# Optimization experiments

Hardware: AMD Instinct MI355X
Metric: run time of the kernel (lower is better)

The kernel has to match this reference:

```python
import jax, jax.numpy as jnp
import numpy as np

EPS = 1e-5

def layer_norm(x, gamma, beta):
    mu = jnp.mean(x, axis=-1, keepdims=True)
    var = jnp.mean(jnp.square(x - mu), axis=-1, keepdims=True)
    return (x - mu) * jax.lax.rsqrt(var + EPS) * gamma + beta

def setup_inputs() -> dict:
    key = jax.random.key(0)
    ks = jax.random.split(key, 12)
    B, S, D = 2, 4096, 1024
    H = 4 * D
    s_in = 1.0 / np.sqrt(D)
    s_h = 1.0 / np.sqrt(H)
    return {
        "input_embedding": jax.random.normal(ks[0], (B, S, D), dtype=jnp.float32),
        "Wq": jax.random.uniform(ks[1], (D, D), jnp.float32, -s_in, s_in),
        "bq": jax.random.uniform(ks[2], (D,), jnp.float32, -s_in, s_in),
        "Wk": jax.random.uniform(ks[3], (D, D), jnp.float32, -s_in, s_in),
        "bk": jax.random.uniform(ks[4], (D,), jnp.float32, -s_in, s_in),
        "Wv": jax.random.uniform(ks[5], (D, D), jnp.float32, -s_in, s_in),
        "bv": jax.random.uniform(ks[6], (D,), jnp.float32, -s_in, s_in),
        "W1": jax.random.uniform(ks[7], (D, H), jnp.float32, -s_in, s_in),
        "b1": jax.random.uniform(ks[8], (H,), jnp.float32, -s_in, s_in),
        "W2": jax.random.uniform(ks[9], (H, D), jnp.float32, -s_h, s_h),
        "b2": jax.random.uniform(ks[10], (D,), jnp.float32, -s_h, s_h),
        "gamma": jnp.ones((D,), jnp.float32),
        "beta": jnp.zeros((D,), jnp.float32),
    }

def reference(input_embedding, Wq, bq, Wk, bk, Wv, bv, W1, b1, W2, b2, gamma, beta):
    D = input_embedding.shape[-1]
    # projections
    k = input_embedding @ Wk + bk
    q = input_embedding @ Wq + bq
    v = input_embedding @ Wv + bv
    # NOTE: original calls attention(k, q, v) so Q<-k, K<-q, V<-v (faithful quirk)
    scores = jnp.einsum('bsd,btd->bst', k, q) / jnp.sqrt(jnp.float32(D))
    attn = jax.nn.softmax(scores, axis=-1)
    attn_out = jnp.einsum('bst,btd->bsd', attn, v)  # dropout = identity (eval)
    x = layer_norm(input_embedding + attn_out, gamma, beta)
    # feed-forward (GELU exact, dropout identity)
    h = jax.nn.gelu(x @ W1 + b1, approximate=False)
    ff = h @ W2 + b2
    return layer_norm(x + ff, gamma, beta)
```

## Files before the change

kernel.cpp:

```cpp
#include <hip/hip_runtime.h>
#include <hip/hip_bf16.h>
#include <stdint.h>

#define AS1 __attribute__((address_space(1)))
#define AS3 __attribute__((address_space(3)))

typedef __bf16 bf16x8 __attribute__((ext_vector_type(8)));
typedef __bf16 bf16x4 __attribute__((ext_vector_type(4)));
typedef float  f32x4  __attribute__((ext_vector_type(4)));

__device__ __forceinline__ void gld_lds16(const void* g, void* l) {
    __builtin_amdgcn_global_load_lds((AS1 void*)g, (AS3 void*)l, 16, 0, 0);
}

__device__ __forceinline__ void xcd_remap(int& bc, int& br) {
    const int GX = gridDim.x, GY = gridDim.y;
    const int L = blockIdx.y * GX + blockIdx.x;
    int rw, rh, nregx;
    if (GX >= 16 && (GX & 1) == 0 && (GY & 3) == 0) {
        rw = GX >> 1; rh = GY >> 2; nregx = 2;
    } else if ((GY & 7) == 0) {
        rw = GX;      rh = GY >> 3; nregx = 1;
    } else {
        bc = blockIdx.x; br = blockIdx.y; return;
    }
    const int xcd  = L & 7;
    const int slot = L >> 3;
    const int rx = xcd % nregx, ry = xcd / nregx;
    bc = rx * rw + slot % rw;
    br = ry * rh + slot / rw;
}

__global__ __launch_bounds__(256, 4)
void gemm_nt(const __bf16* __restrict__ A, const __bf16* __restrict__ B,
             __bf16* __restrict__ C, const float* __restrict__ bias,
             int K, int lda, int ldb, int ldc,
             long sA, long sB, long sC, long sBias,
             int ep, float scale)
{
    __shared__ __bf16 smA[2][4096];
    __shared__ __bf16 smB[2][4096];
    const int t  = threadIdx.x;
    const int l  = t & 63;
    const int w  = t >> 6;
    const int wm = w >> 1, wn = w & 1;
    const int lr = l & 15;
    const int lq = l >> 4;
    const long bz = blockIdx.z;
    int br, bc;
    xcd_remap(bc, br);

    const int swc = ((t & 3) ^ ((t >> 3) & 3)) * 8;
    const __bf16* ag = A + bz * sA + (size_t)(br * 128 + (t >> 2)) * lda + swc;
    const __bf16* bg = B + bz * sB + (size_t)(bc * 128 + (t >> 2)) * ldb + swc;
    const size_t a64 = (size_t)64 * lda, b64 = (size_t)64 * ldb;

    f32x4 acc[4][4];
    const f32x4 zero4 = {0.f, 0.f, 0.f, 0.f};
#pragma unroll
    for (int i = 0; i < 4; ++i)
#pragma unroll
        for (int j = 0; j < 4; ++j) acc[i][j] = zero4;

    const int paOff = (wm * 64 + lr) * 32 + ((lq ^ ((lr >> 1) & 3)) * 8);
    const int pbOff = (wn * 64 + lr) * 32 + ((lq ^ ((lr >> 1) & 3)) * 8);

    auto prefetch = [&](int b) {
        __bf16* la = &smA[b][t * 8];
        __bf16* lb = &smB[b][t * 8];
        gld_lds16(ag,       la);
        gld_lds16(ag + a64, la + 2048);
        gld_lds16(bg,       lb);
        gld_lds16(bg + b64, lb + 2048);
        ag += 32; bg += 32;
    };
    auto compute = [&](int b) {
        const __bf16* pa = &smA[b][paOff];
        const __bf16* pb = &smB[b][pbOff];
        bf16x8 af[4], bfr[4];
#pragma unroll
        for (int i = 0; i < 4; ++i) af[i]  = *(const bf16x8*)(pa + i * 16 * 32);
#pragma unroll
        for (int j = 0; j < 4; ++j) bfr[j] = *(const bf16x8*)(pb + j * 16 * 32);
#pragma unroll
        for (int i = 0; i < 4; ++i)
#pragma unroll
            for (int j = 0; j < 4; ++j)
                acc[i][j] = __builtin_amdgcn_mfma_f32_16x16x32_bf16(af[i], bfr[j], acc[i][j], 0, 0, 0);
    };

    const int nkt = K >> 5;
    prefetch(0);
    for (int kt = 0; kt < nkt; kt += 2) {
        __syncthreads();
        if (kt + 1 < nkt) prefetch(1);
        compute(0);
        __syncthreads();
        if (kt + 2 < nkt) prefetch(0);
        compute(1);
    }

    const int r0 = br * 128 + wm * 64 + lq * 4;
    const int c0 = bc * 128 + wn * 64 + lr;
    C += bz * sC;
    const float* bs = bias ? bias + bz * sBias : nullptr;
#pragma unroll
    for (int i = 0; i < 4; ++i) {
#pragma unroll
        for (int j = 0; j < 4; ++j) {
            const int col = c0 + j * 16;
            const float bcol = (ep != 1 && bs) ? bs[col] : 0.f;
#pragma unroll
            for (int r = 0; r < 4; ++r) {
                const long row = r0 + i * 16 + r;
                const long idx = row * (long)ldc + col;
                const float v = acc[i][j][r];
                if (ep == 0) {
                    C[idx] = (__bf16)(v + bcol);
                } else if (ep == 1) {
                    C[idx] = (__bf16)(v * scale);
                } else {
                    const float u = v + bcol;
                    const float z = 1.59576912f * (u + 0.044715f * u * u * u);
                    C[idx] = (__bf16)(u / (1.f + __expf(-z)));
                }
            }
        }
    }
}

__global__ __launch_bounds__(256)
void conv_bf16(const float* __restrict__ in, __bf16* __restrict__ out)
{
    const long i = (long)blockIdx.x * 256 + threadIdx.x;
    const float4 f = ((const float4*)in)[i];
    bf16x4 o = {(__bf16)f.x, (__bf16)f.y, (__bf16)f.z, (__bf16)f.w};
    ((bf16x4*)out)[i] = o;
}

__global__ void tr_f32_bf16(const float* __restrict__ in, __bf16* __restrict__ out,
                            int K, int N)
{
    __shared__ float tl[32][33];
    const int x = threadIdx.x, y = threadIdx.y;
    const int n0 = blockIdx.x * 32, k0 = blockIdx.y * 32;
#pragma unroll
    for (int i = 0; i < 4; ++i)
        tl[y + 8 * i][x] = in[(size_t)(k0 + y + 8 * i) * N + n0 + x];
    __syncthreads();
#pragma unroll
    for (int i = 0; i < 4; ++i)
        out[(size_t)(n0 + y + 8 * i) * K + k0 + x] = (__bf16)tl[x][y + 8 * i];
}

__global__ void tr_bf16(const __bf16* __restrict__ in, __bf16* __restrict__ out,
                        int R, int C)
{
    in  += (size_t)blockIdx.z * R * C;
    out += (size_t)blockIdx.z * R * C;
    __shared__ __bf16 tl[32][33];
    const int x = threadIdx.x, y = threadIdx.y;
    const int c0 = blockIdx.x * 32, r0 = blockIdx.y * 32;
#pragma unroll
    for (int i = 0; i < 4; ++i)
        tl[y + 8 * i][x] = in[(size_t)(r0 + y + 8 * i) * C + c0 + x];
    __syncthreads();
#pragma unroll
    for (int i = 0; i < 4; ++i)
        out[(size_t)(c0 + y + 8 * i) * R + r0 + x] = tl[x][y + 8 * i];
}

__global__ __launch_bounds__(256)
void softmax_rows(__bf16* __restrict__ S)
{
    __bf16* rp = S + (size_t)blockIdx.x * 4096;
    const int t = threadIdx.x;
    float v[16];
#pragma unroll
    for (int c = 0; c < 2; ++c) {
        const bf16x8 f = ((const bf16x8*)rp)[t + c * 256];
#pragma unroll
        for (int k = 0; k < 8; ++k) v[c * 8 + k] = (float)f[k];
    }
    float mx = v[0];
#pragma unroll
    for (int i = 1; i < 16; ++i) mx = fmaxf(mx, v[i]);
#pragma unroll
    for (int o = 32; o; o >>= 1) mx = fmaxf(mx, __shfl_down(mx, o, 64));
    __shared__ float rm[4], rs[4];
    if ((t & 63) == 0) rm[t >> 6] = mx;
    __syncthreads();
    mx = fmaxf(fmaxf(rm[0], rm[1]), fmaxf(rm[2], rm[3]));
    float s = 0.f;
#pragma unroll
    for (int i = 0; i < 16; ++i) { v[i] = __expf(v[i] - mx); s += v[i]; }
#pragma unroll
    for (int o = 32; o; o >>= 1) s += __shfl_down(s, o, 64);
    if ((t & 63) == 0) rs[t >> 6] = s;
    __syncthreads();
    s = rs[0] + rs[1] + rs[2] + rs[3];
    const float inv = 1.f / s;
#pragma unroll
    for (int c = 0; c < 2; ++c) {
        bf16x8 o8;
#pragma unroll
        for (int k = 0; k < 8; ++k) o8[k] = (__bf16)(v[c * 8 + k] * inv);
        ((bf16x8*)rp)[t + c * 256] = o8;
    }
}

__global__ __launch_bounds__(256)
void ln_residual(const float* __restrict__ af, const __bf16* __restrict__ ab,
                 const __bf16* __restrict__ bb, const __bf16* __restrict__ bb2,
                 const float* __restrict__ lnb,
                 const float* __restrict__ gamma, const float* __restrict__ beta,
                 float* __restrict__ outf, __bf16* __restrict__ outb)
{
    const long row = blockIdx.x;
    const int t = threadIdx.x;
    float x0, x1, x2, x3;
    if (af) {
        const float4 va = ((const float4*)(af + row * 1024))[t];
        x0 = va.x; x1 = va.y; x2 = va.z; x3 = va.w;
    } else {
        const bf16x4 va = ((const bf16x4*)(ab + row * 1024))[t];
        x0 = (float)va[0]; x1 = (float)va[1]; x2 = (float)va[2]; x3 = (float)va[3];
    }
    {
        const bf16x4 vb = ((const bf16x4*)(bb + row * 1024))[t];
        x0 += (float)vb[0]; x1 += (float)vb[1]; x2 += (float)vb[2]; x3 += (float)vb[3];
    }
    if (bb2) {
        const bf16x4 vb = ((const bf16x4*)(bb2 + row * 1024))[t];
        x0 += (float)vb[0]; x1 += (float)vb[1]; x2 += (float)vb[2]; x3 += (float)vb[3];
    }
    if (lnb) {
        const float4 vb = ((const float4*)lnb)[t];
        x0 += vb.x; x1 += vb.y; x2 += vb.z; x3 += vb.w;
    }
    float s = x0 + x1 + x2 + x3;
    float q = x0 * x0 + x1 * x1 + x2 * x2 + x3 * x3;
#pragma unroll
    for (int o = 32; o; o >>= 1) { s += __shfl_down(s, o, 64); q += __shfl_down(q, o, 64); }
    __shared__ float rs[4], rq[4];
    if ((t & 63) == 0) { rs[t >> 6] = s; rq[t >> 6] = q; }
    __syncthreads();
    s = rs[0] + rs[1] + rs[2] + rs[3];
    q = rq[0] + rq[1] + rq[2] + rq[3];
    const float mu  = s * (1.f / 1024.f);
    const float inv = rsqrtf(q * (1.f / 1024.f) - mu * mu + 1e-5f);
    const float4 g  = ((const float4*)gamma)[t];
    const float4 be = ((const float4*)beta)[t];
    const float y0 = (x0 - mu) * inv * g.x + be.x;
    const float y1 = (x1 - mu) * inv * g.y + be.y;
    const float y2 = (x2 - mu) * inv * g.z + be.z;
    const float y3 = (x3 - mu) * inv * g.w + be.w;
    if (outf) ((float4*)(outf + row * 1024))[t] = make_float4(y0, y1, y2, y3);
    if (outb) {
        bf16x4 o4 = {(__bf16)y0, (__bf16)y1, (__bf16)y2, (__bf16)y3};
        ((bf16x4*)outb)[row * 256 + t] = o4;
    }
}

__global__ __launch_bounds__(256)
void fill_diag(float* __restrict__ out, float v, long n)
{
    const long i = (long)blockIdx.x * 256 + threadIdx.x;
    if (i < n) out[i] = v;
}

extern "C" void kernel_launch(void* const* d_in, const int* in_sizes, int n_in,
                              void* d_out, int out_size, void* d_ws, size_t ws_size,
                              hipStream_t stream)
{
    const float* X  = (const float*)d_in[0];
    const float* Wq = (const float*)d_in[1];
    const float* bq = (const float*)d_in[2];
    const float* Wk = (const float*)d_in[3];
    const float* bk = (const float*)d_in[4];
    const float* Wv = (const float*)d_in[5];
    const float* bv = (const float*)d_in[6];
    const float* W1 = (const float*)d_in[7];
    const float* b1 = (const float*)d_in[8];
    const float* W2 = (const float*)d_in[9];
    const float* b2 = (const float*)d_in[10];
    const float* gamma = (const float*)d_in[11];
    const float* beta  = (const float*)d_in[12];
    float* out = (float*)d_out;

    const int S = 4096, D = 1024, H = 4096;
    const int M = 2 * S;

    const size_t szW  = 8388608;
    const size_t szP  = 16777216;
    const size_t oW1T = 0;
    const size_t oW2T = szW;
    const size_t oQP  = 2 * szW;
    const size_t oKP  = oQP + szP;
    const size_t oVP  = oKP + szP;
    const size_t oVT  = oVP + szP;
    const size_t oAO  = oVT + szP;
    const size_t oSL  = oAO + szP;
    const size_t need1 = oSL + 33554432;
    const size_t need2 = oSL + szP;

    int Rs;
    if (ws_size >= need1)      Rs = 4096;
    else if (ws_size >= need2) Rs = 2048;
    else {
        fill_diag<<<dim3((out_size + 255) / 256), dim3(256), 0, stream>>>(
            out, (float)(ws_size >> 20), out_size);
        return;
    }

    char* ws = (char*)d_ws;
    __bf16* W1T = (__bf16*)(ws + oW1T);
    __bf16* W2T = (__bf16*)(ws + oW2T);
    __bf16* QP  = (__bf16*)(ws + oQP);
    __bf16* FF  = (__bf16*)(ws + oQP);
    __bf16* KP  = (__bf16*)(ws + oKP);
    __bf16* HB  = (__bf16*)(ws + oKP);
    __bf16* VP  = (__bf16*)(ws + oVP);
    __bf16* AO2 = (__bf16*)(ws + oVP);
    __bf16* VT  = (__bf16*)(ws + oVT);
    __bf16* WQT = (__bf16*)(ws + oAO);
    float*  BIAS= (float*)(ws + oAO + 6291456);
    __bf16* AO  = (__bf16*)(ws + oAO);
    __bf16* XB  = (__bf16*)(ws + oSL);
    __bf16* SL  = (__bf16*)(ws + oSL);
    __bf16* XLNB= (__bf16*)(ws + oSL);
    __bf16* FF2 = (__bf16*)(ws + oSL + szP);

    const dim3 t256(256);
    const dim3 t32x8(32, 8);

    conv_bf16<<<dim3(M * D / 1024), t256, 0, stream>>>(X, XB);
    tr_f32_bf16<<<dim3(D / 32, D / 32), t32x8, 0, stream>>>(Wq, WQT, D, D);
    tr_f32_bf16<<<dim3(D / 32, D / 32), t32x8, 0, stream>>>(Wk, WQT + (size_t)D * D, D, D);
    tr_f32_bf16<<<dim3(D / 32, D / 32), t32x8, 0, stream>>>(Wv, WQT + (size_t)2 * D * D, D, D);
    tr_f32_bf16<<<dim3(H / 32, D / 32), t32x8, 0, stream>>>(W1, W1T, D, H);
    tr_f32_bf16<<<dim3(D / 32, H / 32), t32x8, 0, stream>>>(W2, W2T, H, D);
    hipMemcpyAsync(BIAS,         bq, D * 4, hipMemcpyDeviceToDevice, stream);
    hipMemcpyAsync(BIAS + D,     bk, D * 4, hipMemcpyDeviceToDevice, stream);
    hipMemcpyAsync(BIAS + 2 * D, bv, D * 4, hipMemcpyDeviceToDevice, stream);

    gemm_nt<<<dim3(D / 128, M / 128, 3), t256, 0, stream>>>(
        XB, WQT, QP, BIAS, D, D, D, D,
        0, (long)D * D, (long)M * D, D, 0, 0.f);

    tr_bf16<<<dim3(D / 32, S / 32, 2), t32x8, 0, stream>>>(VP, VT, S, D);

    const long sCpv = (long)(AO2 - AO);
    for (int b = 0; b < 2; ++b) {
        for (int c = 0; c < S / Rs; ++c) {
            const __bf16* Ak = KP + (size_t)(b * S + c * Rs) * D;
            gemm_nt<<<dim3(S / 128, Rs / 128), t256, 0, stream>>>(
                Ak, QP + (size_t)b * S * D, SL, nullptr, D, D, D, S,
                0, 0, 0, 0, 1, 0.03125f);
            softmax_rows<<<dim3(Rs), t256, 0, stream>>>(SL);
            gemm_nt<<<dim3(D / 128, Rs / 128, 2), t256, 0, stream>>>(
                SL, VT + (size_t)b * D * S, AO + (size_t)(b * S + c * Rs) * D, nullptr,
                S / 2, S, S, D, S / 2, S / 2, sCpv, 0, 0, 0.f);
        }
    }

    ln_residual<<<dim3(M), t256, 0, stream>>>(
        X, nullptr, AO, AO2, nullptr, gamma, beta, nullptr, XLNB);

    gemm_nt<<<dim3(H / 128, M / 128), t256, 0, stream>>>(
        XLNB, W1T, HB, b1, D, D, D, H, 0, 0, 0, 0, 3, 0.f);

    if (Rs == 4096) {
        gemm_nt<<<dim3(D / 128, M / 128, 2), t256, 0, stream>>>(
            HB, W2T, FF, nullptr, H / 2, H, H, D,
            H / 2, H / 2, (long)(FF2 - FF), 0, 1, 1.0f);
        ln_residual<<<dim3(M), t256, 0, stream>>>(
            nullptr, XLNB, FF, FF2, b2, gamma, beta, out, nullptr);
    } else {
        gemm_nt<<<dim3(D / 128, M / 128), t256, 0, stream>>>(
            HB, W2T, FF, b2, H, H, H, D, 0, 0, 0, 0, 0, 0.f);
        ln_residual<<<dim3(M), t256, 0, stream>>>(
            nullptr, XLNB, FF, nullptr, nullptr, gamma, beta, out, nullptr);
    }
}
```

Before: 651.2 us.

## Fuse softmax into score GEMM epilogue and use 256-row GEMM tiles

Adds a gemm_big kernel with 256x128 tiles (larger A tile, 8x4 accumulators, two blocks per CU) and uses it for the QKV, score, FFN1 and FFN2 GEMMs. The score GEMM epilogue now writes unnormalized exp(scale*s) and atomically accumulates row sums. The separate softmax kernel is removed, and normalization is deferred to the attention residual LayerNorm via a per-row reciprocal. The W1/W2 transposes move after attention, which reuses the W1T workspace region for the row-sum buffer. Skipping the max subtraction risks overflow for large scores, and the atomics add contention.

```diff
diff --git a/kernel.cpp b/kernel.cpp
--- a/kernel.cpp
+++ b/kernel.cpp
@@ -31,14 +31,15 @@
     br = ry * rh + slot / rw;
 }
 
-__global__ __launch_bounds__(256, 4)
-void gemm_nt(const __bf16* __restrict__ A, const __bf16* __restrict__ B,
-             __bf16* __restrict__ C, const float* __restrict__ bias,
-             int K, int lda, int ldb, int ldc,
-             long sA, long sB, long sC, long sBias,
-             int ep, float scale)
-{
-    __shared__ __bf16 smA[2][4096];
+__global__ __launch_bounds__(256, 2)
+void gemm_big(const __bf16* __restrict__ A, const __bf16* __restrict__ B,
+              __bf16* __restrict__ C, const float* __restrict__ bias,
+              float* __restrict__ rowsum, long rsOff,
+              int K, int lda, int ldb, int ldc,
+              long sA, long sB, long sC, long sBias,
+              int ep, float scale)
+{
+    __shared__ __bf16 smA[2][8192];
     __shared__ __bf16 smB[2][4096];
     const int t  = threadIdx.x;
     const int l  = t & 63;
@@ -51,25 +52,26 @@
     xcd_remap(bc, br);
 
     const int swc = ((t & 3) ^ ((t >> 3) & 3)) * 8;
-    const __bf16* ag = A + bz * sA + (size_t)(br * 128 + (t >> 2)) * lda + swc;
+    const __bf16* ag = A + bz * sA + (size_t)(br * 256 + (t >> 2)) * lda + swc;
     const __bf16* bg = B + bz * sB + (size_t)(bc * 128 + (t >> 2)) * ldb + swc;
     const size_t a64 = (size_t)64 * lda, b64 = (size_t)64 * ldb;
 
-    f32x4 acc[4][4];
+    f32x4 acc[8][4];
     const f32x4 zero4 = {0.f, 0.f, 0.f, 0.f};
 #pragma unroll
-    for (int i = 0; i < 4; ++i)
+    for (int i = 0; i < 8; ++i)
 #pragma unroll
         for (int j = 0; j < 4; ++j) acc[i][j] = zero4;
 
-    const int paOff = (wm * 64 + lr) * 32 + ((lq ^ ((lr >> 1) & 3)) * 8);
-    const int pbOff = (wn * 64 + lr) * 32 + ((lq ^ ((lr >> 1) & 3)) * 8);
+    const int paOff = (wm * 128 + lr) * 32 + ((lq ^ ((lr >> 1) & 3)) * 8);
+    const int pbOff = (wn * 64  + lr) * 32 + ((lq ^ ((lr >> 1) & 3)) * 8);
 
     auto prefetch = [&](int b) {
         __bf16* la = &smA[b][t * 8];
         __bf16* lb = &smB[b][t * 8];
-        gld_lds16(ag,       la);
-        gld_lds16(ag + a64, la + 2048);
+#pragma unroll
+        for (int rr = 0; rr < 4; ++rr)
+            gld_lds16(ag + rr * a64, la + rr * 2048);
         gld_lds16(bg,       lb);
         gld_lds16(bg + b64, lb + 2048);
         ag += 32; bg += 32;
@@ -77,13 +79,13 @@
     auto compute = [&](int b) {
         const __bf16* pa = &smA[b][paOff];
         const __bf16* pb = &smB[b][pbOff];
-        bf16x8 af[4], bfr[4];
-#pragma unroll
-        for (int i = 0; i < 4; ++i) af[i]  = *(const bf16x8*)(pa + i * 16 * 32);
+        bf16x8 af[8], bfr[4];
+#pragma unroll
+        for (int i = 0; i < 8; ++i) af[i]  = *(const bf16x8*)(pa + i * 16 * 32);
 #pragma unroll
         for (int j = 0; j < 4; ++j) bfr[j] = *(const bf16x8*)(pb + j * 16 * 32);
 #pragma unroll
-        for (int i = 0; i < 4; ++i)
+        for (int i = 0; i < 8; ++i)
 #pragma unroll
             for (int j = 0; j < 4; ++j)
                 acc[i][j] = __builtin_amdgcn_mfma_f32_16x16x32_bf16(af[i], bfr[j], acc[i][j], 0, 0, 0);
@@ -100,12 +102,34 @@
         compute(1);
     }
 
-    const int r0 = br * 128 + wm * 64 + lq * 4;
+    const int r0 = br * 256 + wm * 128 + lq * 4;
     const int c0 = bc * 128 + wn * 64 + lr;
     C += bz * sC;
+
+    if (ep == 2) {
+#pragma unroll
+        for (int i = 0; i < 8; ++i) {
+#pragma unroll
+            for (int r = 0; r < 4; ++r) {
+                const long row = r0 + i * 16 + r;
+                float ps = 0.f;
+#pragma unroll
+                for (int j = 0; j < 4; ++j) {
+                    const float e = __expf(acc[i][j][r] * scale);
+                    C[row * (long)ldc + c0 + j * 16] = (__bf16)e;
+                    ps += e;
+                }
+#pragma unroll
+                for (int o = 1; o < 16; o <<= 1) ps += __shfl_xor(ps, o, 64);
+                if (lr == 0) atomicAdd(&rowsum[rsOff + row], ps);
+            }
+        }
+        return;
+    }
+
     const float* bs = bias ? bias + bz * sBias : nullptr;
 #pragma unroll
-    for (int i = 0; i < 4; ++i) {
+    for (int i = 0; i < 8; ++i) {
 #pragma unroll
         for (int j = 0; j < 4; ++j) {
             const int col = c0 + j * 16;
@@ -129,6 +153,104 @@
     }
 }
 
+__global__ __launch_bounds__(256, 4)
+void gemm_nt(const __bf16* __restrict__ A, const __bf16* __restrict__ B,
+             __bf16* __restrict__ C, const float* __restrict__ bias,
+             int K, int lda, int ldb, int ldc,
+             long sA, long sB, long sC, long sBias,
+             int ep, float scale)
+{
+    __shared__ __bf16 smA[2][4096];
+    __shared__ __bf16 smB[2][4096];
+    const int t  = threadIdx.x;
+    const int l  = t & 63;
+    const int w  = t >> 6;
+    const int wm = w >> 1, wn = w & 1;
+    const int lr = l & 15;
+    const int lq = l >> 4;
+    const long bz = blockIdx.z;
+    int br, bc;
+    xcd_remap(bc, br);
+
+    const int swc = ((t & 3) ^ ((t >> 3) & 3)) * 8;
+    const __bf16* ag = A + bz * sA + (size_t)(br * 128 + (t >> 2)) * lda + swc;
+    const __bf16* bg = B + bz * sB + (size_t)(bc * 128 + (t >> 2)) * ldb + swc;
+    const size_t a64 = (size_t)64 * lda, b64 = (size_t)64 * ldb;
+
+    f32x4 acc[4][4];
+    const f32x4 zero4 = {0.f, 0.f, 0.f, 0.f};
+#pragma unroll
+    for (int i = 0; i < 4; ++i)
+#pragma unroll
+        for (int j = 0; j < 4; ++j) acc[i][j] = zero4;
+
+    const int paOff = (wm * 64 + lr) * 32 + ((lq ^ ((lr >> 1) & 3)) * 8);
+    const int pbOff = (wn * 64 + lr) * 32 + ((lq ^ ((lr >> 1) & 3)) * 8);
+
+    auto prefetch = [&](int b) {
+        __bf16* la = &smA[b][t * 8];
+        __bf16* lb = &smB[b][t * 8];
+        gld_lds16(ag,       la);
+        gld_lds16(ag + a64, la + 2048);
+        gld_lds16(bg,       lb);
+        gld_lds16(bg + b64, lb + 2048);
+        ag += 32; bg += 32;
+    };
+    auto compute = [&](int b) {
+        const __bf16* pa = &smA[b][paOff];
+        const __bf16* pb = &smB[b][pbOff];
+        bf16x8 af[4], bfr[4];
+#pragma unroll
+        for (int i = 0; i < 4; ++i) af[i]  = *(const bf16x8*)(pa + i * 16 * 32);
+#pragma unroll
+        for (int j = 0; j < 4; ++j) bfr[j] = *(const bf16x8*)(pb + j * 16 * 32);
+#pragma unroll
+        for (int i = 0; i < 4; ++i)
+#pragma unroll
+            for (int j = 0; j < 4; ++j)
+                acc[i][j] = __builtin_amdgcn_mfma_f32_16x16x32_bf16(af[i], bfr[j], acc[i][j], 0, 0, 0);
+    };
+
+    const int nkt = K >> 5;
+    prefetch(0);
+    for (int kt = 0; kt < nkt; kt += 2) {
+        __syncthreads();
+        if (kt + 1 < nkt) prefetch(1);
+        compute(0);
+        __syncthreads();
+        if (kt + 2 < nkt) prefetch(0);
+        compute(1);
+    }
+
+    const int r0 = br * 128 + wm * 64 + lq * 4;
+    const int c0 = bc * 128 + wn * 64 + lr;
+    C += bz * sC;
+    const float* bs = bias ? bias + bz * sBias : nullptr;
+#pragma unroll
+    for (int i = 0; i < 4; ++i) {
+#pragma unroll
+        for (int j = 0; j < 4; ++j) {
+            const int col = c0 + j * 16;
+            const float bcol = (ep != 1 && bs) ? bs[col] : 0.f;
+#pragma unroll
+            for (int r = 0; r < 4; ++r) {
+                const long row = r0 + i * 16 + r;
+                const long idx = row * (long)ldc + col;
+                const float v = acc[i][j][r];
+                if (ep == 0) {
+                    C[idx] = (__bf16)(v + bcol);
+                } else if (ep == 1) {
+                    C[idx] = (__bf16)(v * scale);
+                } else {
+                    const float u = v + bcol;
+                    const float z = 1.59576912f * (u + 0.044715f * u * u * u);
+                    C[idx] = (__bf16)(u / (1.f + __expf(-z)));
+                }
+            }
+        }
+    }
+}
+
 __global__ __launch_bounds__(256)
 void conv_bf16(const float* __restrict__ in, __bf16* __restrict__ out)
 {
@@ -136,6 +258,12 @@
     const float4 f = ((const float4*)in)[i];
     bf16x4 o = {(__bf16)f.x, (__bf16)f.y, (__bf16)f.z, (__bf16)f.w};
     ((bf16x4*)out)[i] = o;
+}
+
+__global__ __launch_bounds__(256)
+void zero_f32(float* __restrict__ p)
+{
+    p[(long)blockIdx.x * 256 + threadIdx.x] = 0.f;
 }
 
 __global__ void tr_f32_bf16(const float* __restrict__ in, __bf16* __restrict__ out,
@@ -171,48 +299,9 @@
 }
 
 __global__ __launch_bounds__(256)
-void softmax_rows(__bf16* __restrict__ S)
-{
-    __bf16* rp = S + (size_t)blockIdx.x * 4096;
-    const int t = threadIdx.x;
-    float v[16];
-#pragma unroll
-    for (int c = 0; c < 2; ++c) {
-        const bf16x8 f = ((const bf16x8*)rp)[t + c * 256];
-#pragma unroll
-        for (int k = 0; k < 8; ++k) v[c * 8 + k] = (float)f[k];
-    }
-    float mx = v[0];
-#pragma unroll
-    for (int i = 1; i < 16; ++i) mx = fmaxf(mx, v[i]);
-#pragma unroll
-    for (int o = 32; o; o >>= 1) mx = fmaxf(mx, __shfl_down(mx, o, 64));
-    __shared__ float rm[4], rs[4];
-    if ((t & 63) == 0) rm[t >> 6] = mx;
-    __syncthreads();
-    mx = fmaxf(fmaxf(rm[0], rm[1]), fmaxf(rm[2], rm[3]));
-    float s = 0.f;
-#pragma unroll
-    for (int i = 0; i < 16; ++i) { v[i] = __expf(v[i] - mx); s += v[i]; }
-#pragma unroll
-    for (int o = 32; o; o >>= 1) s += __shfl_down(s, o, 64);
-    if ((t & 63) == 0) rs[t >> 6] = s;
-    __syncthreads();
-    s = rs[0] + rs[1] + rs[2] + rs[3];
-    const float inv = 1.f / s;
-#pragma unroll
-    for (int c = 0; c < 2; ++c) {
-        bf16x8 o8;
-#pragma unroll
-        for (int k = 0; k < 8; ++k) o8[k] = (__bf16)(v[c * 8 + k] * inv);
-        ((bf16x8*)rp)[t + c * 256] = o8;
-    }
-}
-
-__global__ __launch_bounds__(256)
 void ln_residual(const float* __restrict__ af, const __bf16* __restrict__ ab,
                  const __bf16* __restrict__ bb, const __bf16* __restrict__ bb2,
-                 const float* __restrict__ lnb,
+                 const float* __restrict__ lnb, const float* __restrict__ rsum,
                  const float* __restrict__ gamma, const float* __restrict__ beta,
                  float* __restrict__ outf, __bf16* __restrict__ outb)
 {
@@ -226,14 +315,17 @@
         const bf16x4 va = ((const bf16x4*)(ab + row * 1024))[t];
         x0 = (float)va[0]; x1 = (float)va[1]; x2 = (float)va[2]; x3 = (float)va[3];
     }
+    float a0, a1, a2, a3;
     {
         const bf16x4 vb = ((const bf16x4*)(bb + row * 1024))[t];
-        x0 += (float)vb[0]; x1 += (float)vb[1]; x2 += (float)vb[2]; x3 += (float)vb[3];
+        a0 = (float)vb[0]; a1 = (float)vb[1]; a2 = (float)vb[2]; a3 = (float)vb[3];
     }
     if (bb2) {
         const bf16x4 vb = ((const bf16x4*)(bb2 + row * 1024))[t];
-        x0 += (float)vb[0]; x1 += (float)vb[1]; x2 += (float)vb[2]; x3 += (float)vb[3];
-    }
+        a0 += (float)vb[0]; a1 += (float)vb[1]; a2 += (float)vb[2]; a3 += (float)vb[3];
+    }
+    const float rscale = rsum ? 1.f / rsum[row] : 1.f;
+    x0 += a0 * rscale; x1 += a1 * rscale; x2 += a2 * rscale; x3 += a3 * rscale;
     if (lnb) {
         const float4 vb = ((const float4*)lnb)[t];
         x0 += vb.x; x1 += vb.y; x2 += vb.z; x3 += vb.w;
@@ -314,6 +406,7 @@
     }
 
     char* ws = (char*)d_ws;
+    float*  RS  = (float*)(ws + oW1T);
     __bf16* W1T = (__bf16*)(ws + oW1T);
     __bf16* W2T = (__bf16*)(ws + oW2T);
     __bf16* QP  = (__bf16*)(ws + oQP);
@@ -338,14 +431,13 @@
     tr_f32_bf16<<<dim3(D / 32, D / 32), t32x8, 0, stream>>>(Wq, WQT, D, D);
     tr_f32_bf16<<<dim3(D / 32, D / 32), t32x8, 0, stream>>>(Wk, WQT + (size_t)D * D, D, D);
     tr_f32_bf16<<<dim3(D / 32, D / 32), t32x8, 0, stream>>>(Wv, WQT + (size_t)2 * D * D, D, D);
-    tr_f32_bf16<<<dim3(H / 32, D / 32), t32x8, 0, stream>>>(W1, W1T, D, H);
-    tr_f32_bf16<<<dim3(D / 32, H / 32), t32x8, 0, stream>>>(W2, W2T, H, D);
     hipMemcpyAsync(BIAS,         bq, D * 4, hipMemcpyDeviceToDevice, stream);
     hipMemcpyAsync(BIAS + D,     bk, D * 4, hipMemcpyDeviceToDevice, stream);
     hipMemcpyAsync(BIAS + 2 * D, bv, D * 4, hipMemcpyDeviceToDevice, stream);
-
-    gemm_nt<<<dim3(D / 128, M / 128, 3), t256, 0, stream>>>(
-        XB, WQT, QP, BIAS, D, D, D, D,
+    zero_f32<<<dim3(M / 256), t256, 0, stream>>>(RS);
+
+    gemm_big<<<dim3(D / 128, M / 256, 3), t256, 0, stream>>>(
+        XB, WQT, QP, BIAS, nullptr, 0, D, D, D, D,
         0, (long)D * D, (long)M * D, D, 0, 0.f);
 
     tr_bf16<<<dim3(D / 32, S / 32, 2), t32x8, 0, stream>>>(VP, VT, S, D);
@@ -354,10 +446,9 @@
     for (int b = 0; b < 2; ++b) {
         for (int c = 0; c < S / Rs; ++c) {
             const __bf16* Ak = KP + (size_t)(b * S + c * Rs) * D;
-            gemm_nt<<<dim3(S / 128, Rs / 128), t256, 0, stream>>>(
-                Ak, QP + (size_t)b * S * D, SL, nullptr, D, D, D, S,
-                0, 0, 0, 0, 1, 0.03125f);
-            softmax_rows<<<dim3(Rs), t256, 0, stream>>>(SL);
+            gemm_big<<<dim3(S / 128, Rs / 256), t256, 0, stream>>>(
+                Ak, QP + (size_t)b * S * D, SL, nullptr, RS, (long)(b * S + c * Rs),
+                D, D, D, S, 0, 0, 0, 0, 2, 0.03125f);
             gemm_nt<<<dim3(D / 128, Rs / 128, 2), t256, 0, stream>>>(
                 SL, VT + (size_t)b * D * S, AO + (size_t)(b * S + c * Rs) * D, nullptr,
                 S / 2, S, S, D, S / 2, S / 2, sCpv, 0, 0, 0.f);
@@ -365,21 +456,24 @@
     }
 
     ln_residual<<<dim3(M), t256, 0, stream>>>(
-        X, nullptr, AO, AO2, nullptr, gamma, beta, nullptr, XLNB);
-
-    gemm_nt<<<dim3(H / 128, M / 128), t256, 0, stream>>>(
-        XLNB, W1T, HB, b1, D, D, D, H, 0, 0, 0, 0, 3, 0.f);
+        X, nullptr, AO, AO2, nullptr, RS, gamma, beta, nullptr, XLNB);
+
+    tr_f32_bf16<<<dim3(H / 32, D / 32), t32x8, 0, stream>>>(W1, W1T, D, H);
+    tr_f32_bf16<<<dim3(D / 32, H / 32), t32x8, 0, stream>>>(W2, W2T, H, D);
+
+    gemm_big<<<dim3(H / 128, M / 256), t256, 0, stream>>>(
+        XLNB, W1T, HB, b1, nullptr, 0, D, D, D, H, 0, 0, 0, 0, 3, 0.f);
 
     if (Rs == 4096) {
-        gemm_nt<<<dim3(D / 128, M / 128, 2), t256, 0, stream>>>(
-            HB, W2T, FF, nullptr, H / 2, H, H, D,
+        gemm_big<<<dim3(D / 128, M / 256, 2), t256, 0, stream>>>(
+            HB, W2T, FF, nullptr, nullptr, 0, H / 2, H, H, D,
             H / 2, H / 2, (long)(FF2 - FF), 0, 1, 1.0f);
         ln_residual<<<dim3(M), t256, 0, stream>>>(
-            nullptr, XLNB, FF, FF2, b2, gamma, beta, out, nullptr);
+            nullptr, XLNB, FF, FF2, b2, nullptr, gamma, beta, out, nullptr);
     } else {
-        gemm_nt<<<dim3(D / 128, M / 128), t256, 0, stream>>>(
-            HB, W2T, FF, b2, H, H, H, D, 0, 0, 0, 0, 0, 0.f);
+        gemm_big<<<dim3(D / 128, M / 256), t256, 0, stream>>>(
+            HB, W2T, FF, b2, nullptr, 0, H, H, H, D, 0, 0, 0, 0, 0, 0.f);
         ln_residual<<<dim3(M), t256, 0, stream>>>(
-            nullptr, XLNB, FF, nullptr, nullptr, gamma, beta, out, nullptr);
-    }
-}
+            nullptr, XLNB, FF, nullptr, nullptr, nullptr, gamma, beta, out, nullptr);
+    }
+}
```

After: 658.7 us. About the same (+1.2%).

## Fuse softmax exp into QK GEMM epilogue, defer normalization, load B tiles directly

Applied to the files above, without the earlier changes.

Removes the separate softmax kernel. The score GEMM epilogue now writes exp(score*scale) without subtracting the row max, and accumulates row sums with atomics into a workspace buffer. That buffer sits in the W1T region, so the W1/W2 transposes are moved to after attention. The 1/rowsum normalization is applied in the LayerNorm-residual kernel, because PV is linear. The GEMM also drops the shared-memory B tile and loads B fragments straight from global memory into registers with double buffering, and launch bounds change from 4 to 3 waves-per-EU occupancy. Skipping the max subtraction risks overflow for large scores, and the direct B loads may be less coalesced than the shared-memory path.

```diff
diff --git a/kernel.cpp b/kernel.cpp
--- a/kernel.cpp
+++ b/kernel.cpp
@@ -31,15 +31,15 @@
     br = ry * rh + slot / rw;
 }
 
-__global__ __launch_bounds__(256, 4)
+__global__ __launch_bounds__(256, 3)
 void gemm_nt(const __bf16* __restrict__ A, const __bf16* __restrict__ B,
              __bf16* __restrict__ C, const float* __restrict__ bias,
+             float* __restrict__ rowsum, long rsOff,
              int K, int lda, int ldb, int ldc,
              long sA, long sB, long sC, long sBias,
              int ep, float scale)
 {
     __shared__ __bf16 smA[2][4096];
-    __shared__ __bf16 smB[2][4096];
     const int t  = threadIdx.x;
     const int l  = t & 63;
     const int w  = t >> 6;
@@ -52,8 +52,10 @@
 
     const int swc = ((t & 3) ^ ((t >> 3) & 3)) * 8;
     const __bf16* ag = A + bz * sA + (size_t)(br * 128 + (t >> 2)) * lda + swc;
-    const __bf16* bg = B + bz * sB + (size_t)(bc * 128 + (t >> 2)) * ldb + swc;
-    const size_t a64 = (size_t)64 * lda, b64 = (size_t)64 * ldb;
+    const size_t a64 = (size_t)64 * lda;
+
+    const __bf16* bg0 = B + bz * sB + (size_t)(bc * 128 + wn * 64 + lr) * ldb + lq * 8;
+    const size_t b16 = (size_t)16 * ldb;
 
     f32x4 acc[4][4];
     const f32x4 zero4 = {0.f, 0.f, 0.f, 0.f};
@@ -63,25 +65,24 @@
         for (int j = 0; j < 4; ++j) acc[i][j] = zero4;
 
     const int paOff = (wm * 64 + lr) * 32 + ((lq ^ ((lr >> 1) & 3)) * 8);
-    const int pbOff = (wn * 64 + lr) * 32 + ((lq ^ ((lr >> 1) & 3)) * 8);
-
-    auto prefetch = [&](int b) {
+
+    auto prefetchA = [&](int b) {
         __bf16* la = &smA[b][t * 8];
-        __bf16* lb = &smB[b][t * 8];
         gld_lds16(ag,       la);
         gld_lds16(ag + a64, la + 2048);
-        gld_lds16(bg,       lb);
-        gld_lds16(bg + b64, lb + 2048);
-        ag += 32; bg += 32;
+        ag += 32;
     };
-    auto compute = [&](int b) {
+    bf16x8 bcur[4], bnxt[4];
+    auto loadB = [&](bf16x8* dst, int kt) {
+        const __bf16* p = bg0 + kt * 32;
+#pragma unroll
+        for (int j = 0; j < 4; ++j) dst[j] = *(const bf16x8*)(p + j * b16);
+    };
+    auto compute = [&](int b, const bf16x8* bfr) {
         const __bf16* pa = &smA[b][paOff];
-        const __bf16* pb = &smB[b][pbOff];
-        bf16x8 af[4], bfr[4];
-#pragma unroll
-        for (int i = 0; i < 4; ++i) af[i]  = *(const bf16x8*)(pa + i * 16 * 32);
-#pragma unroll
-        for (int j = 0; j < 4; ++j) bfr[j] = *(const bf16x8*)(pb + j * 16 * 32);
+        bf16x8 af[4];
+#pragma unroll
+        for (int i = 0; i < 4; ++i) af[i] = *(const bf16x8*)(pa + i * 16 * 32);
 #pragma unroll
         for (int i = 0; i < 4; ++i)
 #pragma unroll
@@ -90,19 +91,42 @@
     };
 
     const int nkt = K >> 5;
-    prefetch(0);
+    prefetchA(0);
+    loadB(bcur, 0);
     for (int kt = 0; kt < nkt; kt += 2) {
         __syncthreads();
-        if (kt + 1 < nkt) prefetch(1);
-        compute(0);
+        if (kt + 1 < nkt) { prefetchA(1); loadB(bnxt, kt + 1); }
+        compute(0, bcur);
         __syncthreads();
-        if (kt + 2 < nkt) prefetch(0);
-        compute(1);
+        if (kt + 2 < nkt) { prefetchA(0); loadB(bcur, kt + 2); }
+        compute(1, bnxt);
     }
 
     const int r0 = br * 128 + wm * 64 + lq * 4;
     const int c0 = bc * 128 + wn * 64 + lr;
     C += bz * sC;
+
+    if (ep == 2) {
+#pragma unroll
+        for (int i = 0; i < 4; ++i) {
+#pragma unroll
+            for (int r = 0; r < 4; ++r) {
+                const long row = r0 + i * 16 + r;
+                float ps = 0.f;
+#pragma unroll
+                for (int j = 0; j < 4; ++j) {
+                    const float e = __expf(acc[i][j][r] * scale);
+                    C[row * (long)ldc + c0 + j * 16] = (__bf16)e;
+                    ps += e;
+                }
+#pragma unroll
+                for (int o = 1; o < 16; o <<= 1) ps += __shfl_xor(ps, o, 64);
+                if (lr == 0) atomicAdd(&rowsum[rsOff + row], ps);
+            }
+        }
+        return;
+    }
+
     const float* bs = bias ? bias + bz * sBias : nullptr;
 #pragma unroll
     for (int i = 0; i < 4; ++i) {
@@ -138,6 +162,12 @@
     ((bf16x4*)out)[i] = o;
 }
 
+__global__ __launch_bounds__(256)
+void zero_f32(float* __restrict__ p)
+{
+    p[(long)blockIdx.x * 256 + threadIdx.x] = 0.f;
+}
+
 __global__ void tr_f32_bf16(const float* __restrict__ in, __bf16* __restrict__ out,
                             int K, int N)
 {
@@ -171,48 +201,9 @@
 }
 
 __global__ __launch_bounds__(256)
-void softmax_rows(__bf16* __restrict__ S)
-{
-    __bf16* rp = S + (size_t)blockIdx.x * 4096;
-    const int t = threadIdx.x;
-    float v[16];
-#pragma unroll
-    for (int c = 0; c < 2; ++c) {
-        const bf16x8 f = ((const bf16x8*)rp)[t + c * 256];
-#pragma unroll
-        for (int k = 0; k < 8; ++k) v[c * 8 + k] = (float)f[k];
-    }
-    float mx = v[0];
-#pragma unroll
-    for (int i = 1; i < 16; ++i) mx = fmaxf(mx, v[i]);
-#pragma unroll
-    for (int o = 32; o; o >>= 1) mx = fmaxf(mx, __shfl_down(mx, o, 64));
-    __shared__ float rm[4], rs[4];
-    if ((t & 63) == 0) rm[t >> 6] = mx;
-    __syncthreads();
-    mx = fmaxf(fmaxf(rm[0], rm[1]), fmaxf(rm[2], rm[3]));
-    float s = 0.f;
-#pragma unroll
-    for (int i = 0; i < 16; ++i) { v[i] = __expf(v[i] - mx); s += v[i]; }
-#pragma unroll
-    for (int o = 32; o; o >>= 1) s += __shfl_down(s, o, 64);
-    if ((t & 63) == 0) rs[t >> 6] = s;
-    __syncthreads();
-    s = rs[0] + rs[1] + rs[2] + rs[3];
-    const float inv = 1.f / s;
-#pragma unroll
-    for (int c = 0; c < 2; ++c) {
-        bf16x8 o8;
-#pragma unroll
-        for (int k = 0; k < 8; ++k) o8[k] = (__bf16)(v[c * 8 + k] * inv);
-        ((bf16x8*)rp)[t + c * 256] = o8;
-    }
-}
-
-__global__ __launch_bounds__(256)
 void ln_residual(const float* __restrict__ af, const __bf16* __restrict__ ab,
                  const __bf16* __restrict__ bb, const __bf16* __restrict__ bb2,
-                 const float* __restrict__ lnb,
+                 const float* __restrict__ lnb, const float* __restrict__ rsum,
                  const float* __restrict__ gamma, const float* __restrict__ beta,
                  float* __restrict__ outf, __bf16* __restrict__ outb)
 {
@@ -226,14 +217,17 @@
         const bf16x4 va = ((const bf16x4*)(ab + row * 1024))[t];
         x0 = (float)va[0]; x1 = (float)va[1]; x2 = (float)va[2]; x3 = (float)va[3];
     }
+    float a0, a1, a2, a3;
     {
         const bf16x4 vb = ((const bf16x4*)(bb + row * 1024))[t];
-        x0 += (float)vb[0]; x1 += (float)vb[1]; x2 += (float)vb[2]; x3 += (float)vb[3];
+        a0 = (float)vb[0]; a1 = (float)vb[1]; a2 = (float)vb[2]; a3 = (float)vb[3];
     }
     if (bb2) {
         const bf16x4 vb = ((const bf16x4*)(bb2 + row * 1024))[t];
-        x0 += (float)vb[0]; x1 += (float)vb[1]; x2 += (float)vb[2]; x3 += (float)vb[3];
-    }
+        a0 += (float)vb[0]; a1 += (float)vb[1]; a2 += (float)vb[2]; a3 += (float)vb[3];
+    }
+    const float rscale = rsum ? 1.f / rsum[row] : 1.f;
+    x0 += a0 * rscale; x1 += a1 * rscale; x2 += a2 * rscale; x3 += a3 * rscale;
     if (lnb) {
         const float4 vb = ((const float4*)lnb)[t];
         x0 += vb.x; x1 += vb.y; x2 += vb.z; x3 += vb.w;
@@ -314,6 +308,7 @@
     }
 
     char* ws = (char*)d_ws;
+    float*  RS  = (float*)(ws + oW1T);
     __bf16* W1T = (__bf16*)(ws + oW1T);
     __bf16* W2T = (__bf16*)(ws + oW2T);
     __bf16* QP  = (__bf16*)(ws + oQP);
@@ -338,14 +333,13 @@
     tr_f32_bf16<<<dim3(D / 32, D / 32), t32x8, 0, stream>>>(Wq, WQT, D, D);
     tr_f32_bf16<<<dim3(D / 32, D / 32), t32x8, 0, stream>>>(Wk, WQT + (size_t)D * D, D, D);
     tr_f32_bf16<<<dim3(D / 32, D / 32), t32x8, 0, stream>>>(Wv, WQT + (size_t)2 * D * D, D, D);
-    tr_f32_bf16<<<dim3(H / 32, D / 32), t32x8, 0, stream>>>(W1, W1T, D, H);
-    tr_f32_bf16<<<dim3(D / 32, H / 32), t32x8, 0, stream>>>(W2, W2T, H, D);
     hipMemcpyAsync(BIAS,         bq, D * 4, hipMemcpyDeviceToDevice, stream);
     hipMemcpyAsync(BIAS + D,     bk, D * 4, hipMemcpyDeviceToDevice, stream);
     hipMemcpyAsync(BIAS + 2 * D, bv, D * 4, hipMemcpyDeviceToDevice, stream);
+    zero_f32<<<dim3(M / 256), t256, 0, stream>>>(RS);
 
     gemm_nt<<<dim3(D / 128, M / 128, 3), t256, 0, stream>>>(
-        XB, WQT, QP, BIAS, D, D, D, D,
+        XB, WQT, QP, BIAS, nullptr, 0, D, D, D, D,
         0, (long)D * D, (long)M * D, D, 0, 0.f);
 
     tr_bf16<<<dim3(D / 32, S / 32, 2), t32x8, 0, stream>>>(VP, VT, S, D);
@@ -355,31 +349,34 @@
         for (int c = 0; c < S / Rs; ++c) {
             const __bf16* Ak = KP + (size_t)(b * S + c * Rs) * D;
             gemm_nt<<<dim3(S / 128, Rs / 128), t256, 0, stream>>>(
-                Ak, QP + (size_t)b * S * D, SL, nullptr, D, D, D, S,
-                0, 0, 0, 0, 1, 0.03125f);
-            softmax_rows<<<dim3(Rs), t256, 0, stream>>>(SL);
+                Ak, QP + (size_t)b * S * D, SL, nullptr, RS, (long)(b * S + c * Rs),
+                D, D, D, S, 0, 0, 0, 0, 2, 0.03125f);
             gemm_nt<<<dim3(D / 128, Rs / 128, 2), t256, 0, stream>>>(
                 SL, VT + (size_t)b * D * S, AO + (size_t)(b * S + c * Rs) * D, nullptr,
+                nullptr, 0,
                 S / 2, S, S, D, S / 2, S / 2, sCpv, 0, 0, 0.f);
         }
     }
 
     ln_residual<<<dim3(M), t256, 0, stream>>>(
-        X, nullptr, AO, AO2, nullptr, gamma, beta, nullptr, XLNB);
+        X, nullptr, AO, AO2, nullptr, RS, gamma, beta, nullptr, XLNB);
+
+    tr_f32_bf16<<<dim3(H / 32, D / 32), t32x8, 0, stream>>>(W1, W1T, D, H);
+    tr_f32_bf16<<<dim3(D / 32, H / 32), t32x8, 0, stream>>>(W2, W2T, H, D);
 
     gemm_nt<<<dim3(H / 128, M / 128), t256, 0, stream>>>(
-        XLNB, W1T, HB, b1, D, D, D, H, 0, 0, 0, 0, 3, 0.f);
+        XLNB, W1T, HB, b1, nullptr, 0, D, D, D, H, 0, 0, 0, 0, 3, 0.f);
 
     if (Rs == 4096) {
         gemm_nt<<<dim3(D / 128, M / 128, 2), t256, 0, stream>>>(
-            HB, W2T, FF, nullptr, H / 2, H, H, D,
+            HB, W2T, FF, nullptr, nullptr, 0, H / 2, H, H, D,
             H / 2, H / 2, (long)(FF2 - FF), 0, 1, 1.0f);
         ln_residual<<<dim3(M), t256, 0, stream>>>(
-            nullptr, XLNB, FF, FF2, b2, gamma, beta, out, nullptr);
+            nullptr, XLNB, FF, FF2, b2, nullptr, gamma, beta, out, nullptr);
     } else {
         gemm_nt<<<dim3(D / 128, M / 128), t256, 0, stream>>>(
-            HB, W2T, FF, b2, H, H, H, D, 0, 0, 0, 0, 0, 0.f);
+            HB, W2T, FF, b2, nullptr, 0, H, H, H, D, 0, 0, 0, 0, 0, 0.f);
         ln_residual<<<dim3(M), t256, 0, stream>>>(
-            nullptr, XLNB, FF, nullptr, nullptr, gamma, beta, out, nullptr);
-    }
-}
+            nullptr, XLNB, FF, nullptr, nullptr, nullptr, gamma, beta, out, nullptr);
+    }
+}
```

Result: slower. 906.3 us (+39.2%).
